# Kernel tuning notes

Hardware: AMD Instinct MI355X
Metric: run time of the kernel (lower is better)

Reference implementation:

```python
import jax, jax.numpy as jnp
import numpy as np
from jax import lax

K_NEIGH = 20
BN_EPS = 1e-5


def conv2d(x, w, b, pad):
    # x: [B,C,H,W], w: [O,I,kh,kw]
    y = lax.conv_general_dilated(x, w, (1, 1), [(pad, pad), (pad, pad)],
                                 dimension_numbers=('NCHW', 'OIHW', 'NCHW'))
    return y + b[None, :, None, None]


def bn_train(h, gamma, beta):
    # h: [B,N,K,C]; BatchNorm1d in train mode: stats over (B,N,K) per channel
    mean = jnp.mean(h, axis=(0, 1, 2), keepdims=True)
    var = jnp.mean(jnp.square(h - mean), axis=(0, 1, 2), keepdims=True)
    return gamma * (h - mean) * lax.rsqrt(var + BN_EPS) + beta


def edge_conv(F1, w1, b1, g1, bt1, w2, b2, g2, bt2):
    # F1: [B,N,F] with F=1
    B, N, Fd = F1.shape
    sq = jnp.sum(F1 * F1, axis=-1)                               # [B,N]
    dist = sq[:, :, None] + sq[:, None, :] - 2.0 * jnp.einsum('bnf,bmf->bnm', F1, F1)
    idx = jnp.argsort(dist, axis=-1)[:, :, 1:K_NEIGH + 1]        # [B,N,K]
    knn = jax.vmap(lambda xb, ib: xb[ib])(F1, idx)               # [B,N,K,F]
    x1 = jnp.broadcast_to(F1[:, :, None, :], (B, N, K_NEIGH, Fd))
    x_in = jnp.concatenate([x1, knn - x1], axis=-1)              # [B,N,K,2F]
    h = jnp.einsum('bnkc,oc->bnko', x_in, w1) + b1               # 1x1 conv1d
    h = jax.nn.relu(bn_train(h, g1, bt1))
    o = jnp.einsum('bnkc,oc->bnko', h, w2) + b2
    o = jax.nn.relu(bn_train(o, g2, bt2))
    return jnp.max(o, axis=2)                                    # [B,N,an]


def pixel_shuffle(x, r):
    B, C, H, W = x.shape
    x = x.reshape(B, C // (r * r), r, r, H, W)
    x = x.transpose(0, 1, 4, 2, 5, 3)
    return x.reshape(B, C // (r * r), H * r, W * r)


def setup_inputs() -> dict:
    key = jax.random.key(0)
    ks = jax.random.split(key, 8)
    B, H, W = 4, 64, 64
    inp = {
        'x':   jax.random.normal(ks[0], (B, 1, H, W), jnp.float32),
        'c1w': jax.random.normal(ks[1], (64, 1, 5, 5), jnp.float32) * 0.1,
        'c1b': jnp.zeros((64,), jnp.float32),
        'c2w': jax.random.normal(ks[2], (32, 64, 3, 3), jnp.float32) * 0.05,
        'c2b': jnp.zeros((32,), jnp.float32),
        'c3w': jax.random.normal(ks[3], (16, 32, 3, 3), jnp.float32) * 0.05,
        'c3b': jnp.zeros((16,), jnp.float32),
        'c4w': jax.random.normal(ks[4], (1, 16, 3, 3), jnp.float32) * 0.05,
        'c4b': jnp.zeros((1,), jnp.float32),
        'ew1': jax.random.normal(ks[5], (3, 16, 2), jnp.float32) * 0.5,
        'eb1': jnp.zeros((3, 16), jnp.float32),
        'eg1': jnp.ones((3, 16), jnp.float32),
        'ebt1': jnp.zeros((3, 16), jnp.float32),
        'ew2': jax.random.normal(ks[6], (3, 1, 16), jnp.float32) * 0.25,
        'eb2': jnp.zeros((3, 1), jnp.float32),
        'eg2': jnp.ones((3, 1), jnp.float32),
        'ebt2': jnp.zeros((3, 1), jnp.float32),
    }
    return inp


def reference(x, c1w, c1b, c2w, c2b, c3w, c3b, c4w, c4b,
              ew1, eb1, eg1, ebt1, ew2, eb2, eg2, ebt2):
    h = jnp.tanh(conv2d(x, c1w, c1b, 2))
    h = jnp.tanh(conv2d(h, c2w, c2b, 1))
    h = jnp.tanh(conv2d(h, c3w, c3b, 1))
    h = conv2d(h, c4w, c4b, 1)                     # [B,1,H,W]
    B, C, H, W = h.shape
    F1 = h.reshape(B, C, H * W).transpose(0, 2, 1)  # [B,N,1]
    branches = [h]
    for i in range(3):
        o = edge_conv(F1, ew1[i], eb1[i], eg1[i], ebt1[i],
                      ew2[i], eb2[i], eg2[i], ebt2[i])  # [B,N,1]
        branches.append(o.transpose(0, 2, 1).reshape(B, C, H, W))
    p = jnp.concatenate(branches, axis=1)          # [B,4,H,W]
    return jax.nn.sigmoid(pixel_shuffle(p, 2))     # [B,1,2H,2W]
```

## Files before the change

kernel.cpp:

```cpp
#include <hip/hip_runtime.h>
#include <math.h>

#define NPIX 4096
#define KN 20
#define MTOT 327680.0

__device__ inline unsigned long long shflx64(unsigned long long v, int m) {
  unsigned lo = (unsigned)v, hi = (unsigned)(v >> 32);
  lo = __shfl_xor(lo, m, 64);
  hi = __shfl_xor(hi, m, 64);
  return (((unsigned long long)hi) << 32) | lo;
}

__global__ __launch_bounds__(512) void conv12_k(const float* __restrict__ x,
    const float* __restrict__ c1w, const float* __restrict__ c1b,
    const float* __restrict__ c2w, const float* __restrict__ c2b,
    float* __restrict__ part12) {
  __shared__ float sx[224];
  __shared__ float sc1[1920];
  __shared__ float red[4608];
  const int tid = threadIdx.x;
  const int l = tid & 63;
  const int w = __builtin_amdgcn_readfirstlane(tid >> 6);
  const int b = blockIdx.x, tile = blockIdx.y, z = blockIdx.z;
  const int th = (tile >> 3) << 3, tw = (tile & 7) << 3;

  for (int i = tid; i < 196; i += 512) {
    int r = i / 14, c = i - r*14;
    int gr = th - 3 + r, gc = tw - 3 + c;
    sx[r*16 + c] = (gr>=0 && gr<64 && gc>=0 && gc<64) ? x[b*NPIX + (gr<<6) + gc] : 0.f;
  }
  __syncthreads();
  for (int half = 0; half < 2; half++) {
    int px = l + (half << 6);
    if (px < 100) {
      int i = px / 10, j = px - i*10;
      int gy = th - 1 + i, gx = tw - 1 + j;
      bool inb = (gy>=0 && gy<64 && gx>=0 && gx<64);
      for (int cc = 0; cc < 2; cc++) {
        int lc = (w << 1) + cc;
        int co = (z << 4) + lc;
        float acc = c1b[co];
#pragma unroll
        for (int di=0; di<5; di++)
#pragma unroll
          for (int dj=0; dj<5; dj++)
            acc = fmaf(sx[(i+di)*16 + j+dj], c1w[co*25 + di*5 + dj], acc);
        sc1[lc*120 + i*12 + j] = inb ? tanhf(acc) : 0.f;
      }
    }
  }
  __syncthreads();
  float acc[32];
  {
    int py = l >> 3, px2 = l & 7;
#pragma unroll
    for (int o=0;o<32;o++) acc[o] = (z == 0 && w == 0) ? c2b[o] : 0.f;
    for (int ci = 0; ci < 2; ci++) {
      int lc = (w << 1) + ci;
      int cin = (z << 4) + lc;
      const float* sp = sc1 + lc*120;
      float v[9];
#pragma unroll
      for (int di=0;di<3;di++)
#pragma unroll
        for (int dj=0;dj<3;dj++)
          v[di*3+dj] = sp[(py+di)*12 + px2+dj];
      const float* wc = c2w + cin*9;
#pragma unroll
      for (int o=0;o<32;o++) {
        const float* wo = wc + o*576;
#pragma unroll
        for (int t=0;t<9;t++)
          acc[o] = fmaf(v[t], wo[t], acc[o]);
      }
    }
  }
  {
    int py = l >> 3, px2 = l & 7;
    for (int ch = 0; ch < 4; ch++) {
      __syncthreads();
#pragma unroll
      for (int cc = 0; cc < 8; cc++)
        red[w*576 + l*9 + cc] = acc[(ch<<3) + cc];
      __syncthreads();
      float s = red[0*576 + l*9 + w];
#pragma unroll
      for (int ww=1; ww<8; ww++) s += red[ww*576 + l*9 + w];
      int co = (ch<<3) + w;
      part12[(((size_t)(z*4 + b)*32 + co) << 12) + ((th+py)<<6) + (tw+px2)] = s;
    }
  }
}

__global__ __launch_bounds__(512) void conv34_k(const float* __restrict__ part12,
    const float* __restrict__ c3w, const float* __restrict__ c3b,
    const float* __restrict__ c4w, const float* __restrict__ c4b,
    float* __restrict__ fbuf) {
  __shared__ float sc2[3328];
  __shared__ float sc3[1248];
  __shared__ float red[1200];
  const int tid = threadIdx.x;
  const int b = blockIdx.x, tile = blockIdx.y;
  const int th = (tile >> 3) << 2, tw = (tile & 7) << 3;
  const int px = tid & 127;
  const int cinw = __builtin_amdgcn_readfirstlane(tid >> 7);

  for (int i = tid; i < 3072; i += 512) {
    int cin = i / 96, rem = i - cin*96;
    int rr = rem / 12, cc = rem - rr*12;
    int gr = th - 2 + rr, gc = tw - 2 + cc;
    float v = 0.f;
    if (gr>=0 && gr<64 && gc>=0 && gc<64) {
      size_t idx = (((size_t)b*32 + cin) << 12) + (gr<<6) + gc;
      v = tanhf(part12[idx] + part12[idx + 524288] +
                part12[idx + 1048576] + part12[idx + 1572864]);
    }
    sc2[cin*104 + rr*13 + cc] = v;
  }
  __syncthreads();
  float acc[16];
  int pi = px / 10, pj = px - pi*10;
  if (px < 60) {
#pragma unroll
    for (int o=0;o<16;o++) acc[o] = (cinw == 0) ? c3b[o] : 0.f;
    for (int ci = 0; ci < 8; ci++) {
      int cin = (cinw << 3) + ci;
      const float* sp = sc2 + cin*104;
      float v[9];
#pragma unroll
      for (int di=0;di<3;di++)
#pragma unroll
        for (int dj=0;dj<3;dj++)
          v[di*3+dj] = sp[(pi+di)*13 + pj+dj];
      const float* wc = c3w + cin*9;
#pragma unroll
      for (int o=0;o<16;o++) {
        const float* wo = wc + o*288;
#pragma unroll
        for (int t=0;t<9;t++)
          acc[o] = fmaf(v[t], wo[t], acc[o]);
      }
    }
  }
  int gy = th - 1 + pi, gx = tw - 1 + pj;
  bool inb = (gy>=0 && gy<64 && gx>=0 && gx<64);
  for (int ch = 0; ch < 4; ch++) {
    __syncthreads();
    if (px < 60) {
#pragma unroll
      for (int cc = 0; cc < 4; cc++)
        red[cinw*300 + px*5 + cc] = acc[(ch<<2) + cc];
    }
    __syncthreads();
    if (px < 60) {
      float s = red[0*300 + px*5 + cinw];
#pragma unroll
      for (int g=1; g<4; g++) s += red[g*300 + px*5 + cinw];
      int co = (ch<<2) + cinw;
      sc3[co*78 + pi*13 + pj] = inb ? tanhf(s) : 0.f;
    }
  }
  __syncthreads();
  if (tid < 32) {
    int py = tid >> 3, qx = tid & 7;
    float acc4 = c4b[0];
    for (int cin = 0; cin < 16; cin++) {
#pragma unroll
      for (int di=0;di<3;di++)
#pragma unroll
        for (int dj=0;dj<3;dj++)
          acc4 = fmaf(sc3[cin*78 + (py+di)*13 + qx+dj], c4w[cin*9 + di*3+dj], acc4);
    }
    fbuf[b*NPIX + ((th+py)<<6) + (tw+qx)] = acc4;
  }
}

__global__ __launch_bounds__(1024) void sort2_k(const float* __restrict__ f,
    float* __restrict__ sval, int* __restrict__ sidx) {
  int b = blockIdx.x;
  int tid = threadIdx.x;
  int l = tid & 63, w = tid >> 6;
  __shared__ unsigned long long Ab[NPIX];
  __shared__ unsigned long long Bb[NPIX];
  const float* fb = f + b*NPIX;
  unsigned long long key[4];
#pragma unroll
  for (int r=0;r<4;r++) {
    unsigned e = (w<<8) + (r<<6) + l;
    float v = fb[e];
    unsigned u = __float_as_uint(v);
    u ^= (u >> 31) ? 0xFFFFFFFFu : 0x80000000u;
    key[r] = (((unsigned long long)u) << 32) | e;
  }
  for (unsigned k = 2; k <= 256; k <<= 1) {
    for (unsigned j = k >> 1; j > 0; j >>= 1) {
      if (j >= 64) {
        unsigned rj = j >> 6;
#pragma unroll
        for (int r=0;r<4;r++) {
          int pr = r ^ (int)rj;
          if (pr > r) {
            unsigned e = (w<<8)+((unsigned)r<<6)+l;
            bool up = ((e & k & 255u) == 0);
            unsigned long long a = key[r], c = key[pr];
            bool sw = up ? (c < a) : (c > a);
            if (sw) { key[r] = c; key[pr] = a; }
          }
        }
      } else {
#pragma unroll
        for (int r=0;r<4;r++) {
          unsigned e = (w<<8)+((unsigned)r<<6)+l;
          unsigned long long a = key[r];
          unsigned long long p = shflx64(a, (int)j);
          bool up = ((e & k & 255u) == 0);
          bool keepmin = ((e & j) == 0) == up;
          key[r] = (keepmin ? (p < a) : (p > a)) ? p : a;
        }
      }
    }
  }
#pragma unroll
  for (int r=0;r<4;r++) Ab[(w<<8)+(r<<6)+l] = key[r];
  __syncthreads();
  unsigned long long* src = Ab;
  unsigned long long* dst = Bb;
  for (int lg = 8; lg <= 11; lg++) {
    const int L = 1 << lg;
    int p0 = tid << 2;
    int ri = p0 >> lg;
    int base = (ri ^ 1) << lg;
    int mbase = ((ri >> 1) << (lg + 1)) + (p0 & (L - 1));
    unsigned long long kk[4];
    int lo[4], hi[4];
#pragma unroll
    for (int r=0;r<4;r++) { kk[r] = src[p0 + r]; lo[r] = 0; hi[r] = L; }
    for (int s = 0; s <= lg; s++) {
#pragma unroll
      for (int r=0;r<4;r++) {
        if (lo[r] < hi[r]) {
          int mid = (lo[r] + hi[r]) >> 1;
          if (src[base + mid] < kk[r]) lo[r] = mid + 1; else hi[r] = mid;
        }
      }
    }
#pragma unroll
    for (int r=0;r<4;r++) dst[mbase + r + lo[r]] = kk[r];
    __syncthreads();
    unsigned long long* t = src; src = dst; dst = t;
  }
#pragma unroll
  for (int r=0;r<4;r++) {
    int p = (tid << 2) + r;
    unsigned long long kk = src[p];
    unsigned u = (unsigned)(kk >> 32);
    u ^= (u >> 31) ? 0x80000000u : 0xFFFFFFFFu;
    sval[b*NPIX + p] = __uint_as_float(u);
    sidx[b*NPIX + p] = (int)(kk & 0xFFFFFFFFu);
  }
}

__global__ __launch_bounds__(512) void knn4_k(const float* __restrict__ f,
    const float* __restrict__ sval, const int* __restrict__ sidx,
    float* __restrict__ dout, double* __restrict__ part1) {
  const int tid = threadIdx.x, blk = blockIdx.x;
  const int l = tid & 63, w = tid >> 6;
  const int bq = blk >> 7;
  const float* svb = sval + (bq << 12);
  const int*   sib = sidx + (bq << 12);
  const float* fB  = f + (bq << 12);
  double a0=0, a1=0, a2=0, a3=0, a4=0;
  unsigned long long kk[4];
  float fnp[4];
  int   sp[4];
#pragma unroll
  for (int p=0;p<4;p++) {
    int s = ((blk & 127) << 5) + (w << 2) + p;
    sp[p] = s;
    float fn = svb[s]; fnp[p] = fn;
    int start = s - 32;
    if (start < 0) start = 0;
    if (start > NPIX - 64) start = NPIX - 64;
    int q = start + l;
    float fm = svb[q];
    int   m  = sib[q];
    float sqn = __fmul_rn(fn, fn);
    float pr  = __fmul_rn(fn, fm);
    float dist = __fsub_rn(__fadd_rn(sqn, __fmul_rn(fm, fm)), __fmul_rn(2.0f, pr));
    unsigned u = __float_as_uint(dist);
    u ^= (u >> 31) ? 0xFFFFFFFFu : 0x80000000u;
    kk[p] = (((unsigned long long)u) << 32) | (unsigned)m;
  }
#pragma unroll
  for (int k = 2; k <= 64; k <<= 1)
#pragma unroll
    for (int j = k >> 1; j > 0; j >>= 1) {
#pragma unroll
      for (int p=0;p<4;p++) {
        unsigned long long pp = shflx64(kk[p], j);
        bool up = ((l & k) == 0);
        bool keepmin = ((l & j) == 0) == up;
        kk[p] = (keepmin ? (pp < kk[p]) : (pp > kk[p])) ? pp : kk[p];
      }
    }
#pragma unroll
  for (int p=0;p<4;p++) {
    int mr = (int)(kk[p] & 0xFFFFFFFFu);
    float fn = fnp[p];
    float d = __fsub_rn(fB[mr], fn);
    int n = sib[sp[p]];
    if (l >= 1 && l <= 20)
      dout[(size_t)((bq<<12) + n)*KN + (l-1)] = d;
    float dm = (l >= 1 && l <= 20) ? d : 0.f;
    a2 += (double)dm;
    a3 += (double)dm * (double)dm;
    a4 += (double)fn * (double)dm;
    if (l == 0) { a0 += (double)fn; a1 += (double)fn * (double)fn; }
  }
  double v[5] = {a0, a1, a2, a3, a4};
#pragma unroll
  for (int qi=0; qi<5; qi++)
    for (int off=32; off>0; off>>=1) v[qi] += __shfl_down(v[qi], off, 64);
  __shared__ double sred[8][5];
  if (l == 0)
#pragma unroll
    for (int qi=0; qi<5; qi++) sred[w][qi] = v[qi];
  __syncthreads();
  if (tid == 0) {
#pragma unroll
    for (int qi=0; qi<5; qi++) {
      double s = 0.0;
#pragma unroll
      for (int ww=0; ww<8; ww++) s += sred[ww][qi];
      part1[blk*5 + qi] = s;
    }
  }
}

__global__ __launch_bounds__(64) void branch_k(const float* __restrict__ f,
    const float* __restrict__ dw, const double* __restrict__ part1,
    const float* __restrict__ ew1, const float* __restrict__ eb1,
    const float* __restrict__ eg1, const float* __restrict__ ebt1,
    const float* __restrict__ ew2, const float* __restrict__ eb2,
    float* __restrict__ maxo, float* __restrict__ mino,
    double* __restrict__ part2) {
  const int l = threadIdx.x;
  const int blk = blockIdx.x, br = blockIdx.y;
  double a[5] = {0,0,0,0,0};
  for (int b2 = l; b2 < 512; b2 += 64)
#pragma unroll
    for (int q=0;q<5;q++) a[q] += part1[b2*5+q];
#pragma unroll
  for (int q=0;q<5;q++)
    for (int off=32; off>0; off>>=1) a[q] += __shfl_down(a[q], off, 64);
#pragma unroll
  for (int q=0;q<5;q++) a[q] = __shfl(a[q], 0, 64);
  double Ef = a[0]/16384.0, Eff = a[1]/16384.0;
  double Ed = a[2]/MTOT, Edd = a[3]/MTOT, Efd = a[4]/MTOT;
  double Vf = Eff - Ef*Ef, Vd = Edd - Ed*Ed, Cfd = Efd - Ef*Ed;
  float sA[16], sB[16], sC[16], sW[16];
#pragma unroll
  for (int c=0;c<16;c++) {
    int idx = br*16 + c;
    double w0 = (double)ew1[idx*2+0], w1 = (double)ew1[idx*2+1];
    double b1 = (double)eb1[idx];
    double m1 = w0*Ef + w1*Ed + b1;
    double v1 = w0*w0*Vf + 2.0*w0*w1*Cfd + w1*w1*Vd;
    double r1 = 1.0 / sqrt(v1 + 1e-5);
    double g = (double)eg1[idx];
    sA[c] = (float)(g*r1*w0);
    sB[c] = (float)(g*r1*w1);
    sC[c] = (float)(g*r1*(b1 - m1) + (double)ebt1[idx]);
    sW[c] = ew2[idx];
  }
  int row = (blk << 6) + l;
  float fv = f[row];
  const float* dd = dw + (size_t)row*KN;
  float b2v = eb2[br];
  float P[16];
#pragma unroll
  for (int c=0;c<16;c++) P[c] = fmaf(sA[c], fv, sC[c]);
  float mx = -INFINITY, mn = INFINITY;
  double s = 0.0, s2 = 0.0;
  for (int k=0;k<KN;k++) {
    float d = dd[k];
    float t = b2v;
#pragma unroll
    for (int c=0;c<16;c++)
      t = fmaf(sW[c], fmaxf(fmaf(sB[c], d, P[c]), 0.f), t);
    mx = fmaxf(mx, t);
    mn = fminf(mn, t);
    double td = (double)t;
    s += td; s2 += td*td;
  }
  maxo[br*16384 + row] = mx;
  mino[br*16384 + row] = mn;
#pragma unroll
  for (int off=32; off>0; off>>=1) {
    s  += __shfl_down(s, off, 64);
    s2 += __shfl_down(s2, off, 64);
  }
  if (l == 0) {
    part2[(br*256 + blk)*2 + 0] = s;
    part2[(br*256 + blk)*2 + 1] = s2;
  }
}

__global__ __launch_bounds__(256) void out_k(const float* __restrict__ f,
    const float* __restrict__ maxo, const float* __restrict__ mino,
    const double* __restrict__ part2,
    const float* __restrict__ eg2, const float* __restrict__ ebt2,
    float* __restrict__ out) {
  __shared__ float c2c[3][2];
  const int tid = threadIdx.x, blk = blockIdx.x;
  const int l = tid & 63, w = tid >> 6;
  if (w < 3) {
    int br = w;
    double s = 0.0, s2 = 0.0;
#pragma unroll
    for (int i=0;i<4;i++) {
      int bb = l + (i << 6);
      s  += part2[(br*256 + bb)*2 + 0];
      s2 += part2[(br*256 + bb)*2 + 1];
    }
#pragma unroll
    for (int off=32; off>0; off>>=1) {
      s  += __shfl_down(s, off, 64);
      s2 += __shfl_down(s2, off, 64);
    }
    if (l == 0) {
      double mean = s / MTOT;
      double var = s2 / MTOT - mean*mean;
      double r2 = 1.0 / sqrt(var + 1e-5);
      double sc = (double)eg2[br] * r2;
      c2c[br][0] = (float)sc;
      c2c[br][1] = (float)((double)ebt2[br] - sc*mean);
    }
  }
  __syncthreads();
  int tg = (blk << 8) + tid;
  int bo = tg >> 14;
  int y = (tg >> 7) & 127, xx = tg & 127;
  int n = ((y>>1)<<6) + (xx>>1);
  int ch = ((y&1)<<1) + (xx&1);
  float v;
  if (ch == 0) {
    v = f[bo*NPIX + n];
  } else {
    int br = ch - 1;
    float sc = c2c[br][0], sh = c2c[br][1];
    float base = (sc >= 0.f) ? maxo[br*16384 + bo*NPIX + n]
                             : mino[br*16384 + bo*NPIX + n];
    v = fmaxf(fmaf(sc, base, sh), 0.f);
  }
  out[tg] = 1.f / (1.f + expf(-v));
}

extern "C" void kernel_launch(void* const* d_in, const int* in_sizes, int n_in,
                              void* d_out, int out_size, void* d_ws, size_t ws_size,
                              hipStream_t stream) {
  (void)in_sizes; (void)n_in; (void)out_size; (void)ws_size;
  const float* x    = (const float*)d_in[0];
  const float* c1w  = (const float*)d_in[1];
  const float* c1b  = (const float*)d_in[2];
  const float* c2w  = (const float*)d_in[3];
  const float* c2b  = (const float*)d_in[4];
  const float* c3w  = (const float*)d_in[5];
  const float* c3b  = (const float*)d_in[6];
  const float* c4w  = (const float*)d_in[7];
  const float* c4b  = (const float*)d_in[8];
  const float* ew1  = (const float*)d_in[9];
  const float* eb1  = (const float*)d_in[10];
  const float* eg1  = (const float*)d_in[11];
  const float* ebt1 = (const float*)d_in[12];
  const float* ew2  = (const float*)d_in[13];
  const float* eb2  = (const float*)d_in[14];
  const float* eg2  = (const float*)d_in[15];
  const float* ebt2 = (const float*)d_in[16];
  float* out = (float*)d_out;
  float* ws  = (float*)d_ws;

  float*  part12 = ws;
  float*  fbuf  = ws + 2097152;
  float*  dw    = ws + 2113536;
  float*  sval  = ws + 2441216;
  int*    sidx  = (int*)(ws + 2457600);
  float*  maxo  = ws + 2473984;
  float*  mino  = ws + 2523136;
  double* part1 = (double*)(ws + 2572288);
  double* part2 = (double*)(ws + 2577408);

  conv12_k<<<dim3(4,64,4), 512, 0, stream>>>(x, c1w, c1b, c2w, c2b, part12);
  conv34_k<<<dim3(4,128), 512, 0, stream>>>(part12, c3w, c3b, c4w, c4b, fbuf);
  sort2_k<<<4, 1024, 0, stream>>>(fbuf, sval, sidx);
  knn4_k<<<512, 512, 0, stream>>>(fbuf, sval, sidx, dw, part1);
  branch_k<<<dim3(256,3), 64, 0, stream>>>(fbuf, dw, part1,
      ew1, eb1, eg1, ebt1, ew2, eb2, maxo, mino, part2);
  out_k<<<256, 256, 0, stream>>>(fbuf, maxo, mino, part2, eg2, ebt2, out);
}
```

Baseline: 114.5 us.

## Enlarge conv12 tiles to 16x16 and register-block conv2 without shared reduction

New measurement: 104.6 us. 8.7% less time.

```diff
diff --git a/kernel.cpp b/kernel.cpp
--- a/kernel.cpp
+++ b/kernel.cpp
@@ -16,80 +16,76 @@
     const float* __restrict__ c1w, const float* __restrict__ c1b,
     const float* __restrict__ c2w, const float* __restrict__ c2b,
     float* __restrict__ part12) {
-  __shared__ float sx[224];
-  __shared__ float sc1[1920];
-  __shared__ float red[4608];
+  __shared__ float sx[506];
+  __shared__ float sc1[5472];
   const int tid = threadIdx.x;
-  const int l = tid & 63;
-  const int w = __builtin_amdgcn_readfirstlane(tid >> 6);
   const int b = blockIdx.x, tile = blockIdx.y, z = blockIdx.z;
-  const int th = (tile >> 3) << 3, tw = (tile & 7) << 3;
-
-  for (int i = tid; i < 196; i += 512) {
-    int r = i / 14, c = i - r*14;
+  const int th = (tile >> 2) << 4, tw = (tile & 3) << 4;
+
+  for (int i = tid; i < 484; i += 512) {
+    int r = i / 22, c = i - r*22;
     int gr = th - 3 + r, gc = tw - 3 + c;
-    sx[r*16 + c] = (gr>=0 && gr<64 && gc>=0 && gc<64) ? x[b*NPIX + (gr<<6) + gc] : 0.f;
-  }
-  __syncthreads();
-  for (int half = 0; half < 2; half++) {
-    int px = l + (half << 6);
-    if (px < 100) {
-      int i = px / 10, j = px - i*10;
-      int gy = th - 1 + i, gx = tw - 1 + j;
-      bool inb = (gy>=0 && gy<64 && gx>=0 && gx<64);
-      for (int cc = 0; cc < 2; cc++) {
-        int lc = (w << 1) + cc;
-        int co = (z << 4) + lc;
-        float acc = c1b[co];
-#pragma unroll
-        for (int di=0; di<5; di++)
-#pragma unroll
-          for (int dj=0; dj<5; dj++)
-            acc = fmaf(sx[(i+di)*16 + j+dj], c1w[co*25 + di*5 + dj], acc);
-        sc1[lc*120 + i*12 + j] = inb ? tanhf(acc) : 0.f;
+    sx[r*23 + c] = (gr>=0 && gr<64 && gc>=0 && gc<64) ? x[b*NPIX + (gr<<6) + gc] : 0.f;
+  }
+  __syncthreads();
+  for (int idx = tid; idx < 5184; idx += 512) {
+    int co = idx / 324, rem = idx - co*324;
+    int i = rem / 18, j = rem - i*18;
+    int gy = th - 1 + i, gx = tw - 1 + j;
+    bool inb = (gy>=0 && gy<64 && gx>=0 && gx<64);
+    int cg = (z << 4) + co;
+    float acc = c1b[cg];
+#pragma unroll
+    for (int di=0; di<5; di++)
+#pragma unroll
+      for (int dj=0; dj<5; dj++)
+        acc = fmaf(sx[(i+di)*23 + j+dj], c1w[cg*25 + di*5 + dj], acc);
+    sc1[co*342 + i*19 + j] = inb ? tanhf(acc) : 0.f;
+  }
+  __syncthreads();
+  {
+    const int l = tid & 63;
+    const int w = __builtin_amdgcn_readfirstlane(tid >> 6);
+    int row0 = (l >> 4) << 2;
+    int col  = l & 15;
+    int co0 = w << 2;
+    float acc[16];
+#pragma unroll
+    for (int p=0;p<4;p++)
+#pragma unroll
+      for (int q=0;q<4;q++)
+        acc[p*4+q] = (z == 0) ? c2b[co0+q] : 0.f;
+#pragma unroll 2
+    for (int ci = 0; ci < 16; ci++) {
+      const float* sp = sc1 + ci*342;
+      float vb[6][3];
+#pragma unroll
+      for (int r=0;r<6;r++)
+#pragma unroll
+        for (int dj=0;dj<3;dj++)
+          vb[r][dj] = sp[(row0+r)*19 + col + dj];
+      int cin = (z << 4) + ci;
+#pragma unroll
+      for (int q=0;q<4;q++) {
+        const float* wq = c2w + ((size_t)(co0+q)*64 + cin)*9;
+#pragma unroll
+        for (int p=0;p<4;p++) {
+          float a = acc[p*4+q];
+#pragma unroll
+          for (int di=0;di<3;di++)
+#pragma unroll
+            for (int dj=0;dj<3;dj++)
+              a = fmaf(vb[p+di][dj], wq[di*3+dj], a);
+          acc[p*4+q] = a;
+        }
       }
     }
-  }
-  __syncthreads();
-  float acc[32];
-  {
-    int py = l >> 3, px2 = l & 7;
-#pragma unroll
-    for (int o=0;o<32;o++) acc[o] = (z == 0 && w == 0) ? c2b[o] : 0.f;
-    for (int ci = 0; ci < 2; ci++) {
-      int lc = (w << 1) + ci;
-      int cin = (z << 4) + lc;
-      const float* sp = sc1 + lc*120;
-      float v[9];
-#pragma unroll
-      for (int di=0;di<3;di++)
-#pragma unroll
-        for (int dj=0;dj<3;dj++)
-          v[di*3+dj] = sp[(py+di)*12 + px2+dj];
-      const float* wc = c2w + cin*9;
-#pragma unroll
-      for (int o=0;o<32;o++) {
-        const float* wo = wc + o*576;
-#pragma unroll
-        for (int t=0;t<9;t++)
-          acc[o] = fmaf(v[t], wo[t], acc[o]);
-      }
-    }
-  }
-  {
-    int py = l >> 3, px2 = l & 7;
-    for (int ch = 0; ch < 4; ch++) {
-      __syncthreads();
-#pragma unroll
-      for (int cc = 0; cc < 8; cc++)
-        red[w*576 + l*9 + cc] = acc[(ch<<3) + cc];
-      __syncthreads();
-      float s = red[0*576 + l*9 + w];
-#pragma unroll
-      for (int ww=1; ww<8; ww++) s += red[ww*576 + l*9 + w];
-      int co = (ch<<3) + w;
-      part12[(((size_t)(z*4 + b)*32 + co) << 12) + ((th+py)<<6) + (tw+px2)] = s;
-    }
+#pragma unroll
+    for (int q=0;q<4;q++)
+#pragma unroll
+      for (int p=0;p<4;p++)
+        part12[(((size_t)(z*4 + b)*32 + co0+q) << 12)
+               + ((th+row0+p)<<6) + tw + col] = acc[p*4+q];
   }
 }
 
@@ -491,7 +487,7 @@
   double* part1 = (double*)(ws + 2572288);
   double* part2 = (double*)(ws + 2577408);
 
-  conv12_k<<<dim3(4,64,4), 512, 0, stream>>>(x, c1w, c1b, c2w, c2b, part12);
+  conv12_k<<<dim3(4,16,4), 512, 0, stream>>>(x, c1w, c1b, c2w, c2b, part12);
   conv34_k<<<dim3(4,128), 512, 0, stream>>>(part12, c3w, c3b, c4w, c4b, fbuf);
   sort2_k<<<4, 1024, 0, stream>>>(fbuf, sval, sidx);
   knn4_k<<<512, 512, 0, stream>>>(fbuf, sval, sidx, dw, part1);
```
